# Kernel tuning notes

Measured on AMD Instinct MI355X. Metric: run time of the kernel, lower is better.

## Reference

```python
import jax, jax.numpy as jnp
import numpy as np

N, E, G = 50000, 1250000, 256
IN, H, OUT = 64, 64, 2


def _glorot(k, shape):
    fan = shape[0] + shape[1]
    return jax.random.normal(k, shape, jnp.float32) * np.float32(np.sqrt(2.0 / fan))


def setup_inputs() -> dict:
    key = jax.random.key(0)
    ks = jax.random.split(key, 24)
    inp = {
        "x": jax.random.normal(ks[0], (N, IN), jnp.float32),
        "edge_index": jax.random.randint(ks[1], (2, E), 0, N, dtype=jnp.int32),
        "edge_weight": jax.random.uniform(ks[2], (E,), jnp.float32),
        "batch": jnp.sort(jax.random.randint(ks[3], (N,), 0, G, dtype=jnp.int32)),
    }
    # TransformerConv layer 1 (in=IN -> out=H, heads=1, edge_dim=1)
    inp["Wq1"] = _glorot(ks[4], (IN, H)); inp["bq1"] = jnp.zeros((H,), jnp.float32)
    inp["Wk1"] = _glorot(ks[5], (IN, H)); inp["bk1"] = jnp.zeros((H,), jnp.float32)
    inp["Wv1"] = _glorot(ks[6], (IN, H)); inp["bv1"] = jnp.zeros((H,), jnp.float32)
    inp["We1"] = _glorot(ks[7], (1, H))
    inp["Ws1"] = _glorot(ks[8], (IN, H)); inp["bs1"] = jnp.zeros((H,), jnp.float32)
    # TransformerConv layer 2 (H -> H)
    inp["Wq2"] = _glorot(ks[9], (H, H)); inp["bq2"] = jnp.zeros((H,), jnp.float32)
    inp["Wk2"] = _glorot(ks[10], (H, H)); inp["bk2"] = jnp.zeros((H,), jnp.float32)
    inp["Wv2"] = _glorot(ks[11], (H, H)); inp["bv2"] = jnp.zeros((H,), jnp.float32)
    inp["We2"] = _glorot(ks[12], (1, H))
    inp["Ws2"] = _glorot(ks[13], (H, H)); inp["bs2"] = jnp.zeros((H,), jnp.float32)
    # final linear
    inp["Wl"] = _glorot(ks[14], (H, OUT)); inp["bl"] = jnp.zeros((OUT,), jnp.float32)
    return inp


def _tconv(x, src, dst, e_attr, Wq, bq, Wk, bk, Wv, bv, We, Ws, bs, n):
    # PyG TransformerConv, heads=1, concat=True, root_weight=True, beta=False.
    d = Wq.shape[1]
    q = (x @ Wq + bq)[dst]            # [E, d] gather at target nodes
    k = (x @ Wk + bk)[src]            # [E, d] gather at source nodes
    v = (x @ Wv + bv)[src]            # [E, d]
    e = e_attr @ We                   # [E, d] edge embedding (no bias in PyG)
    alpha = jnp.sum(q * (k + e), axis=-1) / jnp.sqrt(jnp.float32(d))  # [E]
    # segment softmax over incoming edges of each target node
    amax = jax.ops.segment_max(alpha, dst, num_segments=n)
    amax = jnp.where(jnp.isfinite(amax), amax, jnp.float32(0.0))
    ex = jnp.exp(alpha - amax[dst])
    denom = jax.ops.segment_sum(ex, dst, num_segments=n)
    w = ex / jnp.maximum(denom[dst], jnp.float32(1e-16))
    out = jax.ops.segment_sum(w[:, None] * (v + e), dst, num_segments=n)  # [n, d]
    return out + x @ Ws + bs          # skip connection (lin_skip)


def reference(x, edge_index, edge_weight, batch,
              Wq1, bq1, Wk1, bk1, Wv1, bv1, We1, Ws1, bs1,
              Wq2, bq2, Wk2, bk2, Wv2, bv2, We2, Ws2, bs2,
              Wl, bl):
    src, dst = edge_index[0], edge_index[1]
    ea = edge_weight[:, None]  # edge_weight.unsqueeze(-1), edge_dim=1
    n = x.shape[0]
    h = jax.nn.relu(_tconv(x, src, dst, ea, Wq1, bq1, Wk1, bk1, Wv1, bv1, We1, Ws1, bs1, n))
    h = jax.nn.relu(_tconv(h, src, dst, ea, Wq2, bq2, Wk2, bk2, Wv2, bv2, We2, Ws2, bs2, n))
    # global_mean_pool over batch ids
    cnt = jax.ops.segment_sum(jnp.ones((n,), jnp.float32), batch, num_segments=G)
    pooled = jax.ops.segment_sum(h, batch, num_segments=G) / jnp.maximum(cnt, 1.0)[:, None]
    return pooled @ Wl + bl
```

## Files before the change

### kernel.cpp

```cpp
#include <hip/hip_runtime.h>
#include <hip/hip_fp16.h>

#define NN 50000
#define NE 1250000
#define NE4 312500
#define NG 256
#define NBKT 196
#define BSH 13
#define BCAP 8192
#define TILE 4096
#define NTB 306

#define QSCALE 0.18033688011112042f
#define EXP2 __builtin_amdgcn_exp2f

#if defined(__has_builtin)
#  if __has_builtin(__builtin_amdgcn_fdot2)
#    define HAS_FDOT2 1
#  endif
#endif

typedef _Float16 h2vec __attribute__((ext_vector_type(2)));

static __device__ __forceinline__ float fdot2f(unsigned a, unsigned b, float c) {
#ifdef HAS_FDOT2
    return __builtin_amdgcn_fdot2(__builtin_bit_cast(h2vec, a),
                                  __builtin_bit_cast(h2vec, b), c, false);
#else
    float2 fa = __half22float2(__builtin_bit_cast(__half2, a));
    float2 fb = __half22float2(__builtin_bit_cast(__half2, b));
    return fmaf(fa.x, fb.x, fmaf(fa.y, fb.y, c));
#endif
}

static __device__ __forceinline__ unsigned h2u(__half2 h) {
    return __builtin_bit_cast(unsigned, h);
}

__global__ void k_zero(int* __restrict__ gCursor) {
    int i = threadIdx.x;
    if (i < NBKT) gCursor[i] = 0;
}

__global__ void k_bscatter(const int* __restrict__ src, const int* __restrict__ dst,
                           const float* __restrict__ ew, int* __restrict__ gCursor,
                           unsigned* __restrict__ bbuf) {
    __shared__ int cnt[NBKT];
    __shared__ int base[NBKT];
    if (threadIdx.x < NBKT) cnt[threadIdx.x] = 0;
    __syncthreads();
    const int4* s4 = (const int4*)src;
    const int4* d4 = (const int4*)dst;
    const float4* w4 = (const float4*)ew;
    int b4 = blockIdx.x * (TILE / 4);
    unsigned rec[16]; int bkt[16];
    #pragma unroll
    for (int j = 0; j < 4; j++) {
        int i4 = b4 + j * 256 + threadIdx.x;
        if (i4 < NE4) {
            int4 s = s4[i4]; int4 d = d4[i4]; float4 w = w4[i4];
            int b0 = d.x >> 8, b1 = d.y >> 8, b2 = d.z >> 8, b3 = d.w >> 8;
            bkt[4*j+0] = b0; bkt[4*j+1] = b1; bkt[4*j+2] = b2; bkt[4*j+3] = b3;
            rec[4*j+0] = (unsigned)s.x | ((unsigned)(d.x & 255) << 16) | ((unsigned)(w.x * 255.f + 0.5f) << 24);
            rec[4*j+1] = (unsigned)s.y | ((unsigned)(d.y & 255) << 16) | ((unsigned)(w.y * 255.f + 0.5f) << 24);
            rec[4*j+2] = (unsigned)s.z | ((unsigned)(d.z & 255) << 16) | ((unsigned)(w.z * 255.f + 0.5f) << 24);
            rec[4*j+3] = (unsigned)s.w | ((unsigned)(d.w & 255) << 16) | ((unsigned)(w.w * 255.f + 0.5f) << 24);
            atomicAdd(&cnt[b0], 1); atomicAdd(&cnt[b1], 1);
            atomicAdd(&cnt[b2], 1); atomicAdd(&cnt[b3], 1);
        } else {
            bkt[4*j+0] = -1; bkt[4*j+1] = -1; bkt[4*j+2] = -1; bkt[4*j+3] = -1;
        }
    }
    __syncthreads();
    if (threadIdx.x < NBKT) {
        int c = cnt[threadIdx.x];
        base[threadIdx.x] = c ? (threadIdx.x << BSH) + atomicAdd(&gCursor[threadIdx.x], c) : 0;
    }
    __syncthreads();
    #pragma unroll
    for (int j = 0; j < 16; j++) {
        if (bkt[j] >= 0) {
            int pos = atomicAdd(&base[bkt[j]], 1);
            if (pos < ((bkt[j] + 1) << BSH)) bbuf[pos] = rec[j];
        }
    }
}

__global__ void k_bsort(const int* __restrict__ gCursor, const unsigned* __restrict__ bbuf,
                        int* __restrict__ off, int* __restrict__ deg,
                        unsigned* __restrict__ pairP) {
    int b = blockIdx.x;
    int st = b << BSH;
    int ce = gCursor[b]; if (ce > BCAP) ce = BCAP;
    __shared__ unsigned sbuf[BCAP];
    __shared__ unsigned sout[BCAP];
    __shared__ int h[256];
    __shared__ int cur[256];
    __shared__ int sscan[256];
    int t = threadIdx.x;
    h[t] = 0;
    __syncthreads();
    for (int i = t; i < ce; i += 256) {
        unsigned r = bbuf[st + i];
        sbuf[i] = r;
        atomicAdd(&h[(r >> 16) & 255], 1);
    }
    __syncthreads();
    int v = h[t];
    sscan[t] = v;
    __syncthreads();
    for (int o = 1; o < 256; o <<= 1) {
        int tmp = (t >= o) ? sscan[t - o] : 0;
        __syncthreads();
        sscan[t] += tmp;
        __syncthreads();
    }
    int exc = sscan[t] - v;
    cur[t] = exc;
    int n = b * 256 + t;
    if (n < NN) { off[n] = st + exc; deg[n] = v; }
    __syncthreads();
    for (int i = t; i < ce; i += 256) {
        unsigned r = sbuf[i];
        int pos = atomicAdd(&cur[(r >> 16) & 255], 1);
        float w = (float)(r >> 24) * (1.f / 255.f);
        unsigned hw = (unsigned)__half_as_ushort(__float2half(w));
        sout[pos] = (r & 0xFFFFu) | (hw << 16);
    }
    __syncthreads();
    for (int i = t; i < ce; i += 256) pairP[st + i] = sout[i];
}

__global__ __launch_bounds__(256, 4)
void k_linear(const float* __restrict__ xin,
              const float* __restrict__ Wq, const float* __restrict__ bq,
              const float* __restrict__ Wk, const float* __restrict__ bk,
              const float* __restrict__ Wv, const float* __restrict__ bv,
              const float* __restrict__ Ws, const float* __restrict__ bs,
              __half* __restrict__ qh, __half* __restrict__ kvh,
              float* __restrict__ agg) {
    int tid = threadIdx.x;
    int mat = tid >> 6, feat = tid & 63;
    const float* W = mat == 0 ? Wq : mat == 1 ? Wk : mat == 2 ? Wv : Ws;
    const float* b = mat == 0 ? bq : mat == 1 ? bk : mat == 2 ? bv : bs;

    float wcol[64];
    #pragma unroll
    for (int k = 0; k < 64; k++) wcol[k] = W[k * 64 + feat];
    float bias = b[feat];
    int kvoff = feat + (mat == 2 ? 64 : 0);

    __shared__ __align__(16) float sx[16 * 64];
    const float4* x4 = (const float4*)xin;

    int n0 = blockIdx.x * 16;
    if (n0 >= NN) return;
    float4 nxt = x4[n0 * 16 + tid];
    int stride = gridDim.x * 16;

    for (; n0 < NN; n0 += stride) {
        __syncthreads();
        ((float4*)sx)[tid] = nxt;
        __syncthreads();
        int n1 = n0 + stride;
        if (n1 < NN) nxt = x4[n1 * 16 + tid];
        for (int c = 0; c < 16; c++) {
            const float4* sxc = (const float4*)(sx + c * 64);
            float a0 = bias, a1 = 0.f, a2 = 0.f, a3 = 0.f;
            #pragma unroll
            for (int k4 = 0; k4 < 16; k4 += 4) {
                float4 v0 = sxc[k4 + 0], v1 = sxc[k4 + 1];
                float4 v2 = sxc[k4 + 2], v3 = sxc[k4 + 3];
                a0 = fmaf(v0.x, wcol[4 * k4 + 0], a0);
                a0 = fmaf(v0.y, wcol[4 * k4 + 1], a0);
                a0 = fmaf(v0.z, wcol[4 * k4 + 2], a0);
                a0 = fmaf(v0.w, wcol[4 * k4 + 3], a0);
                a1 = fmaf(v1.x, wcol[4 * k4 + 4], a1);
                a1 = fmaf(v1.y, wcol[4 * k4 + 5], a1);
                a1 = fmaf(v1.z, wcol[4 * k4 + 6], a1);
                a1 = fmaf(v1.w, wcol[4 * k4 + 7], a1);
                a2 = fmaf(v2.x, wcol[4 * k4 + 8], a2);
                a2 = fmaf(v2.y, wcol[4 * k4 + 9], a2);
                a2 = fmaf(v2.z, wcol[4 * k4 + 10], a2);
                a2 = fmaf(v2.w, wcol[4 * k4 + 11], a2);
                a3 = fmaf(v3.x, wcol[4 * k4 + 12], a3);
                a3 = fmaf(v3.y, wcol[4 * k4 + 13], a3);
                a3 = fmaf(v3.z, wcol[4 * k4 + 14], a3);
                a3 = fmaf(v3.w, wcol[4 * k4 + 15], a3);
            }
            float acc = (a0 + a1) + (a2 + a3);
            int nn = n0 + c;
            if (mat == 0)      qh[nn * 64 + feat] = __float2half(acc * QSCALE);
            else if (mat == 3) agg[nn * 64 + feat] = acc;
            else               kvh[nn * 128 + kvoff] = __float2half(acc);
        }
    }
}

__global__ void k_edge(const unsigned* __restrict__ pairP, const int* __restrict__ off,
                       const int* __restrict__ deg,
                       const __half* __restrict__ qh, const uint4* __restrict__ kv16,
                       const float* __restrict__ We, const float* __restrict__ aggin,
                       float* __restrict__ outp) {
    long gid = (long)blockIdx.x * 256 + threadIdx.x;
    int n = (int)(gid >> 6);
    if (n >= NN) return;
    int lane = threadIdx.x & 63;
    int g = lane >> 3, l = lane & 7;

    const uint4* q4 = (const uint4*)qh;
    uint4 qu = q4[n * 8 + l];
    const float4* wp = (const float4*)(We + l * 8);
    float4 wa = wp[0], wb = wp[1];
    unsigned we01 = h2u(__floats2half2_rn(wa.x, wa.y));
    unsigned we23 = h2u(__floats2half2_rn(wa.z, wa.w));
    unsigned we45 = h2u(__floats2half2_rn(wb.x, wb.y));
    unsigned we67 = h2u(__floats2half2_rn(wb.z, wb.w));

    int st = off[n], dg = deg[n];

    float qwe = fdot2f(qu.x, we01, fdot2f(qu.y, we23,
                fdot2f(qu.z, we45, fdot2f(qu.w, we67, 0.f))));
    qwe += __shfl_xor(qwe, 1); qwe += __shfl_xor(qwe, 2); qwe += __shfl_xor(qwe, 4);

    float den = 0.f, sw = 0.f;
    float acc[8] = {0.f, 0.f, 0.f, 0.f, 0.f, 0.f, 0.f, 0.f};

    auto edge = [&](unsigned pr, uint4 kk, uint4 vv) {
        float w = __half2float(__ushort_as_half((unsigned short)(pr >> 16)));
        float tA = fdot2f(qu.x, kk.x, fdot2f(qu.y, kk.y, 0.f));
        float tB = fdot2f(qu.z, kk.z, fdot2f(qu.w, kk.w, 0.f));
        float t = tA + tB;
        t += __shfl_xor(t, 1); t += __shfl_xor(t, 2); t += __shfl_xor(t, 4);
        t = fmaf(w, qwe, t);
        float p = EXP2(t);
        den += p;
        sw = fmaf(p, w, sw);
        float2 v0 = __half22float2(__builtin_bit_cast(__half2, vv.x));
        float2 v1 = __half22float2(__builtin_bit_cast(__half2, vv.y));
        float2 v2 = __half22float2(__builtin_bit_cast(__half2, vv.z));
        float2 v3 = __half22float2(__builtin_bit_cast(__half2, vv.w));
        acc[0] = fmaf(p, v0.x, acc[0]); acc[1] = fmaf(p, v0.y, acc[1]);
        acc[2] = fmaf(p, v1.x, acc[2]); acc[3] = fmaf(p, v1.y, acc[3]);
        acc[4] = fmaf(p, v2.x, acc[4]); acc[5] = fmaf(p, v2.y, acc[5]);
        acc[6] = fmaf(p, v3.x, acc[6]); acc[7] = fmaf(p, v3.y, acc[7]);
    };

    int nfull = dg >> 3;
    if (nfull > 0) {
        unsigned prA = pairP[st + g];
        unsigned prB = (nfull > 1) ? pairP[st + 8 + g] : 0u;
        unsigned rowA = prA & 0xFFFFu;
        uint4 kkA = kv16[rowA * 16 + l];
        uint4 vvA = kv16[rowA * 16 + 8 + l];
        for (int i = 0; i + 1 < nfull; i++) {
            unsigned prC = (i + 2 < nfull) ? pairP[st + (i + 2) * 8 + g] : 0u;
            unsigned rowB = prB & 0xFFFFu;
            uint4 kkB = kv16[rowB * 16 + l];
            uint4 vvB = kv16[rowB * 16 + 8 + l];
            edge(prA, kkA, vvA);
            prA = prB; kkA = kkB; vvA = vvB; prB = prC;
        }
        edge(prA, kkA, vvA);
    }
    int tl = nfull * 8 + g;
    if (tl < dg) {
        unsigned pr = pairP[st + tl];
        unsigned row = pr & 0xFFFFu;
        uint4 kk = kv16[row * 16 + l];
        uint4 vv = kv16[row * 16 + 8 + l];
        edge(pr, kk, vv);
    }

    #pragma unroll
    for (int o = 8; o <= 32; o <<= 1) {
        den += __shfl_xor(den, o);
        sw  += __shfl_xor(sw, o);
        #pragma unroll
        for (int j = 0; j < 8; j++) acc[j] += __shfl_xor(acc[j], o);
    }

    if (g == 0) {
        float inv = 1.f / fmaxf(den, 1e-16f);
        float swi = sw * inv;
        const float4* ain = (const float4*)(aggin + n * 64 + l * 8);
        float4 a0 = ain[0], a1 = ain[1];
        a0.x = fmaxf(fmaf(acc[0], inv, fmaf(swi, wa.x, a0.x)), 0.f);
        a0.y = fmaxf(fmaf(acc[1], inv, fmaf(swi, wa.y, a0.y)), 0.f);
        a0.z = fmaxf(fmaf(acc[2], inv, fmaf(swi, wa.z, a0.z)), 0.f);
        a0.w = fmaxf(fmaf(acc[3], inv, fmaf(swi, wa.w, a0.w)), 0.f);
        a1.x = fmaxf(fmaf(acc[4], inv, fmaf(swi, wb.x, a1.x)), 0.f);
        a1.y = fmaxf(fmaf(acc[5], inv, fmaf(swi, wb.y, a1.y)), 0.f);
        a1.z = fmaxf(fmaf(acc[6], inv, fmaf(swi, wb.z, a1.z)), 0.f);
        a1.w = fmaxf(fmaf(acc[7], inv, fmaf(swi, wb.w, a1.w)), 0.f);
        float4* ao = (float4*)(outp + n * 64 + l * 8);
        ao[0] = a0; ao[1] = a1;
    }
}

__global__ void k_final(const float* __restrict__ h, const int* __restrict__ batch,
                        const float* __restrict__ Wl, const float* __restrict__ bl,
                        float* __restrict__ out) {
    int g = blockIdx.x;
    int tid = threadIdx.x;
    int lo = 0, hi = NN;
    while (lo < hi) { int mid = (lo + hi) >> 1; if (batch[mid] < g) lo = mid + 1; else hi = mid; }
    int s0 = lo;
    hi = NN;
    while (lo < hi) { int mid = (lo + hi) >> 1; if (batch[mid] < g + 1) lo = mid + 1; else hi = mid; }
    int s1 = lo;

    int sub = tid >> 6, lane = tid & 63;
    float a = 0.f;
    for (int n = s0 + sub; n < s1; n += 4) a += h[n * 64 + lane];
    __shared__ float sred[4][64];
    sred[sub][lane] = a;
    __syncthreads();
    if (tid < 64) {
        float p = (sred[0][tid] + sred[1][tid] + sred[2][tid] + sred[3][tid])
                  / fmaxf((float)(s1 - s0), 1.f);
        float a0 = p * Wl[tid * 2 + 0];
        float a1 = p * Wl[tid * 2 + 1];
        #pragma unroll
        for (int o = 1; o < 64; o <<= 1) { a0 += __shfl_xor(a0, o); a1 += __shfl_xor(a1, o); }
        if (tid == 0) { out[g * 2 + 0] = a0 + bl[0]; out[g * 2 + 1] = a1 + bl[1]; }
    }
}

extern "C" void kernel_launch(void* const* d_in, const int* in_sizes, int n_in,
                              void* d_out, int out_size, void* d_ws, size_t ws_size,
                              hipStream_t stream) {
    const float* x    = (const float*)d_in[0];
    const int*   ei   = (const int*)d_in[1];
    const float* ew   = (const float*)d_in[2];
    const int*   batch= (const int*)d_in[3];
    const float *Wq1 = (const float*)d_in[4],  *bq1 = (const float*)d_in[5],
                *Wk1 = (const float*)d_in[6],  *bk1 = (const float*)d_in[7],
                *Wv1 = (const float*)d_in[8],  *bv1 = (const float*)d_in[9],
                *We1 = (const float*)d_in[10], *Ws1 = (const float*)d_in[11],
                *bs1 = (const float*)d_in[12],
                *Wq2 = (const float*)d_in[13], *bq2 = (const float*)d_in[14],
                *Wk2 = (const float*)d_in[15], *bk2 = (const float*)d_in[16],
                *Wv2 = (const float*)d_in[17], *bv2 = (const float*)d_in[18],
                *We2 = (const float*)d_in[19], *Ws2 = (const float*)d_in[20],
                *bs2 = (const float*)d_in[21],
                *Wl  = (const float*)d_in[22], *bl  = (const float*)d_in[23];
    const int* src = ei;
    const int* dst = ei + NE;
    float* out = (float*)d_out;

    float* p = (float*)d_ws;
    float* agg1 = p; p += (size_t)NN * 64;
    float* agg2 = p; p += (size_t)NN * 64;
    __half* qh  = (__half*)p; p += (size_t)NN * 32;
    __half* kvh = (__half*)p; p += (size_t)NN * 64;
    unsigned* bbuf  = (unsigned*)p; p += (size_t)NBKT * BCAP;
    unsigned* pairP = (unsigned*)p; p += (size_t)NBKT * BCAP;
    int* gCursor = (int*)p; p += NBKT;
    int* off     = (int*)p; p += NN;
    int* deg     = (int*)p; p += NN;

    dim3 b256(256);
    int wgrid = (int)(((long)NN * 64 + 255) / 256);

    k_zero<<<1, b256, 0, stream>>>(gCursor);
    k_bscatter<<<NTB, b256, 0, stream>>>(src, dst, ew, gCursor, bbuf);
    k_bsort<<<NBKT, b256, 0, stream>>>(gCursor, bbuf, off, deg, pairP);

    k_linear<<<1024, b256, 0, stream>>>(x, Wq1, bq1, Wk1, bk1, Wv1, bv1, Ws1, bs1,
                                        qh, kvh, agg1);
    k_edge<<<wgrid, b256, 0, stream>>>(pairP, off, deg, qh, (const uint4*)kvh, We1,
                                       agg1, agg1);

    k_linear<<<1024, b256, 0, stream>>>(agg1, Wq2, bq2, Wk2, bk2, Wv2, bv2, Ws2, bs2,
                                        qh, kvh, agg2);
    k_edge<<<wgrid, b256, 0, stream>>>(pairP, off, deg, qh, (const uint4*)kvh, We2,
                                       agg2, agg2);

    k_final<<<NG, b256, 0, stream>>>(agg2, batch, Wl, bl, out);
}
```

Before: 209.0 us.

## Compute two weight matrices per thread in k_linear and tile 32 nodes per block

```diff
diff --git a/kernel.cpp b/kernel.cpp
--- a/kernel.cpp
+++ b/kernel.cpp
@@ -131,7 +131,7 @@
     for (int i = t; i < ce; i += 256) pairP[st + i] = sout[i];
 }
 
-__global__ __launch_bounds__(256, 4)
+__global__ __launch_bounds__(256, 2)
 void k_linear(const float* __restrict__ xin,
               const float* __restrict__ Wq, const float* __restrict__ bq,
               const float* __restrict__ Wk, const float* __restrict__ bk,
@@ -140,59 +140,84 @@
               __half* __restrict__ qh, __half* __restrict__ kvh,
               float* __restrict__ agg) {
     int tid = threadIdx.x;
-    int mat = tid >> 6, feat = tid & 63;
-    const float* W = mat == 0 ? Wq : mat == 1 ? Wk : mat == 2 ? Wv : Ws;
-    const float* b = mat == 0 ? bq : mat == 1 ? bk : mat == 2 ? bv : bs;
-
-    float wcol[64];
+    int wid = tid >> 6;
+    int sub = wid >> 1;
+    int mp  = wid & 1;
+    int feat = tid & 63;
+    const float* W0 = mp == 0 ? Wq : Wv;
+    const float* B0 = mp == 0 ? bq : bv;
+    const float* W1 = mp == 0 ? Wk : Ws;
+    const float* B1 = mp == 0 ? bk : bs;
+
+    float w0[64], w1[64];
     #pragma unroll
-    for (int k = 0; k < 64; k++) wcol[k] = W[k * 64 + feat];
-    float bias = b[feat];
-    int kvoff = feat + (mat == 2 ? 64 : 0);
-
-    __shared__ __align__(16) float sx[16 * 64];
+    for (int k = 0; k < 64; k++) {
+        w0[k] = W0[k * 64 + feat];
+        w1[k] = W1[k * 64 + feat];
+    }
+    float bias0 = B0[feat], bias1 = B1[feat];
+
+    __shared__ __align__(16) float sx[32 * 64];
     const float4* x4 = (const float4*)xin;
-
-    int n0 = blockIdx.x * 16;
+    const int NF4 = NN * 16;
+    float4 z = make_float4(0.f, 0.f, 0.f, 0.f);
+
+    int n0 = blockIdx.x * 32;
     if (n0 >= NN) return;
-    float4 nxt = x4[n0 * 16 + tid];
-    int stride = gridDim.x * 16;
+    int stride = gridDim.x * 32;
+    int i0 = n0 * 16 + tid;
+    float4 nxt0 = (i0 < NF4) ? x4[i0] : z;
+    float4 nxt1 = (i0 + 256 < NF4) ? x4[i0 + 256] : z;
 
     for (; n0 < NN; n0 += stride) {
         __syncthreads();
-        ((float4*)sx)[tid] = nxt;
+        ((float4*)sx)[tid] = nxt0;
+        ((float4*)sx)[tid + 256] = nxt1;
         __syncthreads();
         int n1 = n0 + stride;
-        if (n1 < NN) nxt = x4[n1 * 16 + tid];
+        if (n1 < NN) {
+            int j0 = n1 * 16 + tid;
+            nxt0 = (j0 < NF4) ? x4[j0] : z;
+            nxt1 = (j0 + 256 < NF4) ? x4[j0 + 256] : z;
+        }
+        int nb = n0 + sub * 16;
+        const float* sxb = sx + sub * 16 * 64;
         for (int c = 0; c < 16; c++) {
-            const float4* sxc = (const float4*)(sx + c * 64);
-            float a0 = bias, a1 = 0.f, a2 = 0.f, a3 = 0.f;
+            int nn = nb + c;
+            if (nn >= NN) break;
+            const float4* sxc = (const float4*)(sxb + c * 64);
+            float a0 = bias0, a1 = 0.f, a2 = 0.f, a3 = 0.f;
+            float c0 = bias1, c1 = 0.f, c2 = 0.f, c3 = 0.f;
             #pragma unroll
             for (int k4 = 0; k4 < 16; k4 += 4) {
                 float4 v0 = sxc[k4 + 0], v1 = sxc[k4 + 1];
                 float4 v2 = sxc[k4 + 2], v3 = sxc[k4 + 3];
-                a0 = fmaf(v0.x, wcol[4 * k4 + 0], a0);
-                a0 = fmaf(v0.y, wcol[4 * k4 + 1], a0);
-                a0 = fmaf(v0.z, wcol[4 * k4 + 2], a0);
-                a0 = fmaf(v0.w, wcol[4 * k4 + 3], a0);
-                a1 = fmaf(v1.x, wcol[4 * k4 + 4], a1);
-                a1 = fmaf(v1.y, wcol[4 * k4 + 5], a1);
-                a1 = fmaf(v1.z, wcol[4 * k4 + 6], a1);
-                a1 = fmaf(v1.w, wcol[4 * k4 + 7], a1);
-                a2 = fmaf(v2.x, wcol[4 * k4 + 8], a2);
-                a2 = fmaf(v2.y, wcol[4 * k4 + 9], a2);
-                a2 = fmaf(v2.z, wcol[4 * k4 + 10], a2);
-                a2 = fmaf(v2.w, wcol[4 * k4 + 11], a2);
-                a3 = fmaf(v3.x, wcol[4 * k4 + 12], a3);
-                a3 = fmaf(v3.y, wcol[4 * k4 + 13], a3);
-                a3 = fmaf(v3.z, wcol[4 * k4 + 14], a3);
-                a3 = fmaf(v3.w, wcol[4 * k4 + 15], a3);
+                a0 = fmaf(v0.x, w0[4 * k4 + 0], a0);  c0 = fmaf(v0.x, w1[4 * k4 + 0], c0);
+                a0 = fmaf(v0.y, w0[4 * k4 + 1], a0);  c0 = fmaf(v0.y, w1[4 * k4 + 1], c0);
+                a0 = fmaf(v0.z, w0[4 * k4 + 2], a0);  c0 = fmaf(v0.z, w1[4 * k4 + 2], c0);
+                a0 = fmaf(v0.w, w0[4 * k4 + 3], a0);  c0 = fmaf(v0.w, w1[4 * k4 + 3], c0);
+                a1 = fmaf(v1.x, w0[4 * k4 + 4], a1);  c1 = fmaf(v1.x, w1[4 * k4 + 4], c1);
+                a1 = fmaf(v1.y, w0[4 * k4 + 5], a1);  c1 = fmaf(v1.y, w1[4 * k4 + 5], c1);
+                a1 = fmaf(v1.z, w0[4 * k4 + 6], a1);  c1 = fmaf(v1.z, w1[4 * k4 + 6], c1);
+                a1 = fmaf(v1.w, w0[4 * k4 + 7], a1);  c1 = fmaf(v1.w, w1[4 * k4 + 7], c1);
+                a2 = fmaf(v2.x, w0[4 * k4 + 8], a2);  c2 = fmaf(v2.x, w1[4 * k4 + 8], c2);
+                a2 = fmaf(v2.y, w0[4 * k4 + 9], a2);  c2 = fmaf(v2.y, w1[4 * k4 + 9], c2);
+                a2 = fmaf(v2.z, w0[4 * k4 + 10], a2); c2 = fmaf(v2.z, w1[4 * k4 + 10], c2);
+                a2 = fmaf(v2.w, w0[4 * k4 + 11], a2); c2 = fmaf(v2.w, w1[4 * k4 + 11], c2);
+                a3 = fmaf(v3.x, w0[4 * k4 + 12], a3); c3 = fmaf(v3.x, w1[4 * k4 + 12], c3);
+                a3 = fmaf(v3.y, w0[4 * k4 + 13], a3); c3 = fmaf(v3.y, w1[4 * k4 + 13], c3);
+                a3 = fmaf(v3.z, w0[4 * k4 + 14], a3); c3 = fmaf(v3.z, w1[4 * k4 + 14], c3);
+                a3 = fmaf(v3.w, w0[4 * k4 + 15], a3); c3 = fmaf(v3.w, w1[4 * k4 + 15], c3);
             }
-            float acc = (a0 + a1) + (a2 + a3);
-            int nn = n0 + c;
-            if (mat == 0)      qh[nn * 64 + feat] = __float2half(acc * QSCALE);
-            else if (mat == 3) agg[nn * 64 + feat] = acc;
-            else               kvh[nn * 128 + kvoff] = __float2half(acc);
+            float acc0 = (a0 + a1) + (a2 + a3);
+            float acc1 = (c0 + c1) + (c2 + c3);
+            if (mp == 0) {
+                qh[nn * 64 + feat] = __float2half(acc0 * QSCALE);
+                kvh[nn * 128 + feat] = __float2half(acc1);
+            } else {
+                kvh[nn * 128 + 64 + feat] = __float2half(acc0);
+                agg[nn * 64 + feat] = acc1;
+            }
         }
     }
 }
@@ -362,18 +387,19 @@
 
     dim3 b256(256);
     int wgrid = (int)(((long)NN * 64 + 255) / 256);
+    int lgrid = (NN + 63) / 64;
 
     k_zero<<<1, b256, 0, stream>>>(gCursor);
     k_bscatter<<<NTB, b256, 0, stream>>>(src, dst, ew, gCursor, bbuf);
     k_bsort<<<NBKT, b256, 0, stream>>>(gCursor, bbuf, off, deg, pairP);
 
-    k_linear<<<1024, b256, 0, stream>>>(x, Wq1, bq1, Wk1, bk1, Wv1, bv1, Ws1, bs1,
-                                        qh, kvh, agg1);
+    k_linear<<<lgrid, b256, 0, stream>>>(x, Wq1, bq1, Wk1, bk1, Wv1, bv1, Ws1, bs1,
+                                         qh, kvh, agg1);
     k_edge<<<wgrid, b256, 0, stream>>>(pairP, off, deg, qh, (const uint4*)kvh, We1,
                                        agg1, agg1);
 
-    k_linear<<<1024, b256, 0, stream>>>(agg1, Wq2, bq2, Wk2, bk2, Wv2, bv2, Ws2, bs2,
-                                        qh, kvh, agg2);
+    k_linear<<<lgrid, b256, 0, stream>>>(agg1, Wq2, bq2, Wk2, bk2, Wv2, bv2, Ws2, bs2,
+                                         qh, kvh, agg2);
     k_edge<<<wgrid, b256, 0, stream>>>(pairP, off, deg, qh, (const uint4*)kvh, We2,
                                        agg2, agg2);
 
```

Result: slower. 234.9 us (+12.4%).
